# Performance work log

Measured on AMD Instinct MI355X. Metric: run time of the kernel, lower is better.

Reference implementation:

```python
import jax, jax.numpy as jnp
import numpy as np

D_MODEL = 1024
NHEAD = 16
DHEAD = D_MODEL // NHEAD
DFF = 4096
B, S = 2, 2048
R = 25                # local_attention_radius = 5*5
K = 5                 # rel_pos_max_distance
W = 2 * R + 1         # window width
EPS = 1e-5


def setup_inputs() -> dict:
    key = jax.random.key(0)
    ks = jax.random.split(key, 12)
    s = 0.02
    g = lambda k, shape: jax.random.normal(k, shape, jnp.float32) * s
    return {
        "src": jax.random.normal(ks[0], (B, S, D_MODEL), jnp.float32),
        # attention in/out projections (W stored [out,in], applied x @ W.T + b)
        "wq": g(ks[1], (D_MODEL, D_MODEL)), "bq": jnp.zeros((D_MODEL,), jnp.float32),
        "wk": g(ks[2], (D_MODEL, D_MODEL)), "bk": jnp.zeros((D_MODEL,), jnp.float32),
        "wv": g(ks[3], (D_MODEL, D_MODEL)), "bv": jnp.zeros((D_MODEL,), jnp.float32),
        "wo": g(ks[4], (D_MODEL, D_MODEL)), "bo": jnp.zeros((D_MODEL,), jnp.float32),
        # relative position embeddings, ids clipped to [-K, K] -> 2K+1 rows
        "rel_emb": g(ks[5], (2 * K + 1, DHEAD)),
        # FFN
        "w1": g(ks[6], (DFF, D_MODEL)), "b1": jnp.zeros((DFF,), jnp.float32),
        "w2": g(ks[7], (D_MODEL, DFF)), "b2": jnp.zeros((D_MODEL,), jnp.float32),
        # layernorms
        "g1": jnp.ones((D_MODEL,), jnp.float32), "beta1": jnp.zeros((D_MODEL,), jnp.float32),
        "g2": jnp.ones((D_MODEL,), jnp.float32), "beta2": jnp.zeros((D_MODEL,), jnp.float32),
    }


def _layernorm(x, g, b):
    m = x.mean(-1, keepdims=True)
    v = ((x - m) ** 2).mean(-1, keepdims=True)
    return (x - m) * jax.lax.rsqrt(v + EPS) * g + b


def _rel_window_attention(x, wq, bq, wk, bk, wv, bv, wo, bo, rel_emb):
    b, s, d = x.shape

    def proj(w, bias):
        return (x @ w.T + bias).reshape(b, s, NHEAD, DHEAD).transpose(0, 2, 1, 3)

    q = proj(wq, bq)  # [B,H,S,Dh]
    k = proj(wk, bk)
    v = proj(wv, bv)

    offsets = jnp.arange(-R, R + 1)                     # [W]
    j = jnp.arange(s)[:, None] + offsets[None, :]       # [S,W] absolute key index
    valid = (j >= 0) & (j < s)
    jc = jnp.clip(j, 0, s - 1)

    scale = 1.0 / np.sqrt(DHEAD).astype(np.float32)
    k_win = k[:, :, jc]                                 # [B,H,S,W,Dh] banded gather
    scores = jnp.einsum('bhsd,bhswd->bhsw', q, k_win) * scale
    rel_ids = jnp.clip(offsets, -K, K) + K              # [W]
    scores = scores + jnp.einsum('bhsd,wd->bhsw', q, rel_emb[rel_ids]) * scale
    scores = jnp.where(valid[None, None], scores, jnp.float32(-1e30))
    attn = jax.nn.softmax(scores, axis=-1)              # [B,H,S,W]

    v_win = v[:, :, jc]                                 # [B,H,S,W,Dh]
    out = jnp.einsum('bhsw,bhswd->bhsd', attn, v_win)
    out = out.transpose(0, 2, 1, 3).reshape(b, s, d)
    return out @ wo.T + bo


def reference(src, wq, bq, wk, bk, wv, bv, wo, bo, rel_emb,
              w1, b1, w2, b2, g1, beta1, g2, beta2):
    # post-norm (norm_first=False default) transformer block, dropout=0 (eval)
    z = _rel_window_attention(src, wq, bq, wk, bk, wv, bv, wo, bo, rel_emb)
    x = _layernorm(src + z, g1, beta1)
    ff = jax.nn.relu(x @ w1.T + b1) @ w2.T + b2
    return _layernorm(x + ff, g2, beta2)
```

## Files before the change

kernel.cpp:

```cpp
#include <hip/hip_runtime.h>


#define D_MODEL 1024
#define SEQ     2048
#define NROWS   4096
#define WIN     51
#define RAD     25

typedef __attribute__((ext_vector_type(8))) __bf16 bf16x8;
typedef __attribute__((ext_vector_type(4))) float  floatx4;

__device__ __forceinline__ unsigned short f2bf(float x) {
    unsigned u = __float_as_uint(x);
    unsigned r = u + 0x7fffu + ((u >> 16) & 1u);
    return (unsigned short)(r >> 16);
}
__device__ __forceinline__ float bf2f(unsigned short h) {
    return __uint_as_float(((unsigned)h) << 16);
}

__device__ __forceinline__ void gld16(const unsigned short* g, unsigned short* l) {
    __builtin_amdgcn_global_load_lds(
        (const __attribute__((address_space(1))) unsigned int*)g,
        (__attribute__((address_space(3))) unsigned int*)l,
        16, 0, 0);
}

__device__ __forceinline__ void cvtgrp(const float* __restrict__ in,
                                       unsigned short* __restrict__ out, int g) {
    float4 f = ((const float4*)in)[g];
    ushort4 u;
    u.x = f2bf(f.x); u.y = f2bf(f.y); u.z = f2bf(f.z); u.w = f2bf(f.w);
    ((ushort4*)out)[g] = u;
}

__global__ __launch_bounds__(256)
void cvt_all(const float* __restrict__ src,
             const float* __restrict__ wq, const float* __restrict__ wk,
             const float* __restrict__ wv, const float* __restrict__ wo,
             const float* __restrict__ w1, const float* __restrict__ w2,
             const float* __restrict__ bq, const float* __restrict__ bk,
             const float* __restrict__ bv,
             unsigned short* __restrict__ xb,
             unsigned short* __restrict__ wqkvb,
             unsigned short* __restrict__ wob,
             unsigned short* __restrict__ w1b,
             unsigned short* __restrict__ w2b,
             float* __restrict__ bqkv)
{
    int g = blockIdx.x * 256 + threadIdx.x;
    if (g >= 4194496) return;
    if (g < 1048576) { cvtgrp(src, xb, g); return; }
    g -= 1048576;
    if (g < 262144) { cvtgrp(wq, wqkvb, g); return; }
    g -= 262144;
    if (g < 262144) { cvtgrp(wk, wqkvb + 1048576, g); return; }
    g -= 262144;
    if (g < 262144) { cvtgrp(wv, wqkvb + 2097152, g); return; }
    g -= 262144;
    if (g < 262144) { cvtgrp(wo, wob, g); return; }
    g -= 262144;
    if (g < 1048576) { cvtgrp(w1, w1b, g); return; }
    g -= 1048576;
    if (g < 1048576) { cvtgrp(w2, w2b, g); return; }
    g -= 1048576;
    float4 f = (g < 64) ? ((const float4*)bq)[g]
             : (g < 128) ? ((const float4*)bk)[g - 64]
                         : ((const float4*)bv)[g - 128];
    ((float4*)bqkv)[g] = f;
}

#define ROT3(x) ((x) == 16384 ? 0 : (x) + 8192)

__global__ __launch_bounds__(512, 2)
void gemm256(const unsigned short* __restrict__ A,
             const unsigned short* __restrict__ Wt,
             const float* __restrict__ bias,
             unsigned short* __restrict__ Cb,
             int kstride, int kloop, int T, int tncnt,
             int ldc, int relu, size_t sstep1, size_t sstep2)
{
    __shared__ __attribute__((aligned(16))) unsigned short AS[3 * 8192];
    __shared__ __attribute__((aligned(16))) unsigned short BS[3 * 8192];

    const int id = blockIdx.x;
    const int s  = id / T;
    const int t0 = id - s * T;
    const int sid = (t0 & 7) * (T >> 3) + (t0 >> 3);
    const int bm = (sid / tncnt) * 256;
    const int bn = (sid % tncnt) * 256;

    const int tid  = threadIdx.x;
    const int lane = tid & 63;
    const int wave = tid >> 6;
    const int wr   = wave >> 2;
    const int wc   = wave & 3;
    const int fm   = lane & 15;
    const int fq   = lane >> 4;

    const int kofs = s * kloop;
    const int NT   = kloop >> 5;

    const int ks  = (tid >> 3) & 7;
    const int gi  = tid ^ ks;
    const int r0s = gi >> 2;
    const int c2s = gi & 3;
    const unsigned short* Agp = A  + (size_t)(bm + r0s) * kstride + kofs + c2s * 8;
    const unsigned short* Wgp = Wt + (size_t)(bn + r0s) * kstride + kofs + c2s * 8;
    const size_t istep = (size_t)128 * kstride;

    const int rA  = wr * 128 + fm;
    const int rB  = wc * 64  + fm;
    const int c0A = ((((rA << 2) | fq) ^ (fm >> 1)) << 3);
    const int c0B = ((((rB << 2) | fq) ^ (fm >> 1)) << 3);

    gld16(Agp,              AS + tid * 8);
    gld16(Agp + istep,      AS + tid * 8 + 4096);
    gld16(Wgp,              BS + tid * 8);
    gld16(Wgp + istep,      BS + tid * 8 + 4096);
    gld16(Agp + 32,         AS + 8192 + tid * 8);
    gld16(Agp + 32 + istep, AS + 8192 + tid * 8 + 4096);
    gld16(Wgp + 32,         BS + 8192 + tid * 8);
    gld16(Wgp + 32 + istep, BS + 8192 + tid * 8 + 4096);
    asm volatile("s_waitcnt vmcnt(4)" ::: "memory");
    __builtin_amdgcn_sched_barrier(0);
    __builtin_amdgcn_s_barrier();
    __builtin_amdgcn_sched_barrier(0);

    floatx4 acc[8][4] = {};
    const unsigned short* Aga = Agp + 64;
    const unsigned short* Wga = Wgp + 64;
    int cb = 0;
    int pb = 16384;

    for (int t = 0; t < NT; t++) {
        const bool pf = (t + 2 < NT);

        bf16x8 af0[4], bfr[4];
        #pragma unroll
        for (int mi = 0; mi < 4; mi++)
            af0[mi] = *(const bf16x8*)(AS + cb + c0A + mi * 512);
        #pragma unroll
        for (int ni = 0; ni < 4; ni++)
            bfr[ni] = *(const bf16x8*)(BS + cb + c0B + ni * 512);
        if (pf) {
            gld16(Aga,         AS + pb + tid * 8);
            gld16(Aga + istep, AS + pb + tid * 8 + 4096);
        }
        __builtin_amdgcn_sched_barrier(0);
        __builtin_amdgcn_s_barrier();
        __builtin_amdgcn_sched_barrier(0);
        __builtin_amdgcn_s_setprio(1);
        #pragma unroll
        for (int mi = 0; mi < 4; mi++)
            #pragma unroll
            for (int ni = 0; ni < 4; ni++)
                acc[mi][ni] = __builtin_amdgcn_mfma_f32_16x16x32_bf16(
                    af0[mi], bfr[ni], acc[mi][ni], 0, 0, 0);
        __builtin_amdgcn_s_setprio(0);
        __builtin_amdgcn_sched_barrier(0);
        __builtin_amdgcn_s_barrier();
        __builtin_amdgcn_sched_barrier(0);

        bf16x8 af1[4];
        #pragma unroll
        for (int mi = 0; mi < 4; mi++)
            af1[mi] = *(const bf16x8*)(AS + cb + c0A + (mi + 4) * 512);
        if (pf) {
            gld16(Wga,         BS + pb + tid * 8);
            gld16(Wga + istep, BS + pb + tid * 8 + 4096);
        }
        __builtin_amdgcn_sched_barrier(0);
        __builtin_amdgcn_s_barrier();
        __builtin_amdgcn_sched_barrier(0);
        __builtin_amdgcn_s_setprio(1);
        #pragma unroll
        for (int mi = 0; mi < 4; mi++)
            #pragma unroll
            for (int ni = 0; ni < 4; ni++)
                acc[mi + 4][ni] = __builtin_amdgcn_mfma_f32_16x16x32_bf16(
                    af1[mi], bfr[ni], acc[mi + 4][ni], 0, 0, 0);
        __builtin_amdgcn_s_setprio(0);

        if (t + 1 < NT) {
            if (pf) asm volatile("s_waitcnt vmcnt(4)" ::: "memory");
            else    asm volatile("s_waitcnt vmcnt(0)" ::: "memory");
            __builtin_amdgcn_sched_barrier(0);
            __builtin_amdgcn_s_barrier();
            __builtin_amdgcn_sched_barrier(0);
        }
        cb = ROT3(cb);
        pb = ROT3(pb);
        Aga += 32;
        Wga += 32;
    }

    unsigned short* Co = Cb + (size_t)(s & 1) * sstep1 + (size_t)(s >> 1) * sstep2;
    const int r0  = bm + wr * 128 + fq * 4;
    const int c0e = bn + wc * 64 + fm;
    #pragma unroll
    for (int mi = 0; mi < 8; mi++) {
        #pragma unroll
        for (int ni = 0; ni < 4; ni++) {
            const int col = c0e + ni * 16;
            const float bv = bias ? bias[col] : 0.0f;
            #pragma unroll
            for (int rr = 0; rr < 4; rr++) {
                const int row = r0 + mi * 16 + rr;
                float v = acc[mi][ni][rr] + bv;
                if (relu) v = fmaxf(v, 0.0f);
                Co[(size_t)row * ldc + col] = f2bf(v);
            }
        }
    }
}

__global__ __launch_bounds__(256, 2)
void attn_mfma(const unsigned short* __restrict__ qkv,
               const float* __restrict__ rel,
               unsigned short* __restrict__ attnb)
{
    __shared__ __attribute__((aligned(16))) unsigned short Qs[64 * 72];
    __shared__ __attribute__((aligned(16))) unsigned short Ks[128 * 72];
    __shared__ __attribute__((aligned(16))) unsigned short Vt[64 * 168];
    __shared__ __attribute__((aligned(16))) unsigned short Rs[16 * 72];
    __shared__ __attribute__((aligned(16))) unsigned short Pl[4 * 16 * 104];
    __shared__ float Qrl[4 * 16 * 12];

    const int t   = threadIdx.x;
    const int blk = blockIdx.x;
    const int st  = blk & 31;
    const int h   = (blk >> 5) & 15;
    const int b   = blk >> 9;
    const int s0  = st << 6;
    const int brow0 = b * SEQ;

    const int trow = t >> 3;
    const int tc   = (t & 7) * 8;
    const uint4 z4 = make_uint4(0, 0, 0, 0);

    #pragma unroll
    for (int p = 0; p < 2; p++) {
        int r = trow + p * 32;
        uint4 v = *(const uint4*)(qkv + (size_t)(brow0 + s0 + r) * 3072 + h * 64 + tc);
        *(uint4*)(Qs + r * 72 + tc) = v;
    }
    #pragma unroll
    for (int p = 0; p < 4; p++) {
        int kr = trow + p * 32;
        int ka = s0 - 25 + kr;
        bool in = (ka >= 0) & (ka < SEQ);
        uint4 kv = z4, vv = z4;
        if (in) {
            kv = *(const uint4*)(qkv + (size_t)(brow0 + ka) * 3072 + 1024 + h * 64 + tc);
            vv = *(const uint4*)(qkv + (size_t)(brow0 + ka) * 3072 + 2048 + h * 64 + tc);
        }
        *(uint4*)(Ks + kr * 72 + tc) = kv;
        const unsigned short* e = (const unsigned short*)&vv;
        #pragma unroll
        for (int j = 0; j < 8; j++)
            Vt[(tc + j) * 168 + kr] = e[j];
    }
    if (t < 176) {
        float4 f = ((const float4*)rel)[t];
        int fi = t * 4, rr = fi >> 6, cc = fi & 63;
        ushort4 u;
        u.x = f2bf(f.x); u.y = f2bf(f.y); u.z = f2bf(f.z); u.w = f2bf(f.w);
        *(ushort4*)(Rs + rr * 72 + cc) = u;
    } else {
        int fi = 704 + (t - 176) * 4, rr = fi >> 6, cc = fi & 63;
        *(ushort4*)(Rs + rr * 72 + cc) = make_ushort4(0, 0, 0, 0);
    }
    {
        int n = t * 4, w2 = n >> 8, rem = n & 255, rr = rem >> 4, cc = 80 + (rem & 15);
        *(ushort4*)(Pl + w2 * (16 * 104) + rr * 104 + cc) = make_ushort4(0, 0, 0, 0);
    }
    for (int idx = t; idx < 320; idx += 256) {
        int r = idx / 5, cchunk = idx % 5;
        *(uint4*)(Vt + r * 168 + 128 + cchunk * 8) = z4;
    }
    __syncthreads();

    const int wave = t >> 6;
    const int lane = t & 63;
    const int fm   = lane & 15;
    const int fk8  = (lane >> 4) * 8;
    const int S0w  = s0 + wave * 16;
    unsigned short* Plw = Pl + wave * (16 * 104);
    float* Ql = Qrl + wave * (16 * 12);

    bf16x8 qa0 = *(const bf16x8*)(Qs + (wave * 16 + fm) * 72 + fk8);
    bf16x8 qa1 = *(const bf16x8*)(Qs + (wave * 16 + fm) * 72 + fk8 + 32);

    floatx4 Sc[5];
    #pragma unroll
    for (int nt = 0; nt < 5; nt++) {
        bf16x8 kb0 = *(const bf16x8*)(Ks + (wave * 16 + nt * 16 + fm) * 72 + fk8);
        bf16x8 kb1 = *(const bf16x8*)(Ks + (wave * 16 + nt * 16 + fm) * 72 + fk8 + 32);
        floatx4 acc = {0.f, 0.f, 0.f, 0.f};
        acc = __builtin_amdgcn_mfma_f32_16x16x32_bf16(qa0, kb0, acc, 0, 0, 0);
        acc = __builtin_amdgcn_mfma_f32_16x16x32_bf16(qa1, kb1, acc, 0, 0, 0);
        Sc[nt] = acc;
    }
    {
        bf16x8 rb0 = *(const bf16x8*)(Rs + fm * 72 + fk8);
        bf16x8 rb1 = *(const bf16x8*)(Rs + fm * 72 + fk8 + 32);
        floatx4 qr = {0.f, 0.f, 0.f, 0.f};
        qr = __builtin_amdgcn_mfma_f32_16x16x32_bf16(qa0, rb0, qr, 0, 0, 0);
        qr = __builtin_amdgcn_mfma_f32_16x16x32_bf16(qa1, rb1, qr, 0, 0, 0);
        if (fm < 12) {
            #pragma unroll
            for (int reg = 0; reg < 4; reg++)
                Ql[((lane >> 4) * 4 + reg) * 12 + fm] = qr[reg];
        }
    }

    float inv[4];
    const int iq0 = (lane >> 4) * 4;
    #pragma unroll
    for (int reg = 0; reg < 4; reg++) {
        const int i = iq0 + reg;
        float sc[5];
        float mx = -1e30f;
        #pragma unroll
        for (int nt = 0; nt < 5; nt++) {
            int c   = nt * 16 + fm;
            int off = c - 25 - i;
            int ka  = S0w - 25 + c;
            bool valid = (off >= -RAD) & (off <= RAD) & (ka >= 0) & (ka < SEQ);
            int rid = min(max(off, -5), 5) + 5;
            float v = valid ? (Sc[nt][reg] + Ql[i * 12 + rid]) * 0.125f : -1e30f;
            sc[nt] = v;
            mx = fmaxf(mx, v);
        }
        #pragma unroll
        for (int o = 1; o < 16; o <<= 1) mx = fmaxf(mx, __shfl_xor(mx, o));
        float sum = 0.f;
        #pragma unroll
        for (int nt = 0; nt < 5; nt++) {
            float e = __expf(sc[nt] - mx);
            sum += e;
            Plw[i * 104 + nt * 16 + fm] = f2bf(e);
        }
        #pragma unroll
        for (int o = 1; o < 16; o <<= 1) sum += __shfl_xor(sum, o);
        inv[reg] = 1.0f / sum;
    }

    floatx4 O[4] = {};
    #pragma unroll
    for (int kc = 0; kc < 3; kc++) {
        bf16x8 pa = *(const bf16x8*)(Plw + fm * 104 + fk8 + kc * 32);
        #pragma unroll
        for (int nt = 0; nt < 4; nt++) {
            bf16x8 vb = *(const bf16x8*)(Vt + (nt * 16 + fm) * 168 + wave * 16 + fk8 + kc * 32);
            O[nt] = __builtin_amdgcn_mfma_f32_16x16x32_bf16(pa, vb, O[nt], 0, 0, 0);
        }
    }

    #pragma unroll
    for (int nt = 0; nt < 4; nt++) {
        const int d = nt * 16 + fm;
        #pragma unroll
        for (int reg = 0; reg < 4; reg++) {
            const int i = iq0 + reg;
            attnb[(size_t)(brow0 + S0w + i) * 1024 + h * 64 + d] = f2bf(O[nt][reg] * inv[reg]);
        }
    }
}

__global__ __launch_bounds__(256)
void ln_fuse(const float* __restrict__ resf,
             const unsigned short* __restrict__ resb,
             const unsigned short* __restrict__ p0,
             const unsigned short* __restrict__ p1,
             const unsigned short* __restrict__ p2,
             const unsigned short* __restrict__ p3,
             const float* __restrict__ cbias,
             const float* __restrict__ gamma,
             const float* __restrict__ beta,
             float* __restrict__ outf,
             unsigned short* __restrict__ outb)
{
    const int wave = threadIdx.x >> 6;
    const int lane = threadIdx.x & 63;
    const int row = blockIdx.x * 4 + wave;
    const size_t base = (size_t)row * D_MODEL;

    float x[16];
    float sum = 0.0f, sq = 0.0f;
    #pragma unroll
    for (int i = 0; i < 4; i++) {
        const int c4 = lane + i * 64;
        ushort4 u0 = ((const ushort4*)(p0 + base))[c4];
        ushort4 u1 = ((const ushort4*)(p1 + base))[c4];
        float4 cb = ((const float4*)cbias)[c4];
        float4 va;
        if (resf) {
            va = ((const float4*)(resf + base))[c4];
        } else {
            ushort4 ua = ((const ushort4*)(resb + base))[c4];
            va.x = bf2f(ua.x); va.y = bf2f(ua.y); va.z = bf2f(ua.z); va.w = bf2f(ua.w);
        }
        float e0 = va.x + bf2f(u0.x) + bf2f(u1.x) + cb.x;
        float e1 = va.y + bf2f(u0.y) + bf2f(u1.y) + cb.y;
        float e2 = va.z + bf2f(u0.z) + bf2f(u1.z) + cb.z;
        float e3 = va.w + bf2f(u0.w) + bf2f(u1.w) + cb.w;
        if (p2) {
            ushort4 u2 = ((const ushort4*)(p2 + base))[c4];
            ushort4 u3 = ((const ushort4*)(p3 + base))[c4];
            e0 += bf2f(u2.x) + bf2f(u3.x);
            e1 += bf2f(u2.y) + bf2f(u3.y);
            e2 += bf2f(u2.z) + bf2f(u3.z);
            e3 += bf2f(u2.w) + bf2f(u3.w);
        }
        x[i*4+0] = e0; x[i*4+1] = e1; x[i*4+2] = e2; x[i*4+3] = e3;
        sum += e0 + e1 + e2 + e3;
        sq  += e0*e0 + e1*e1 + e2*e2 + e3*e3;
    }
    #pragma unroll
    for (int off = 32; off > 0; off >>= 1) {
        sum += __shfl_xor(sum, off);
        sq  += __shfl_xor(sq,  off);
    }
    const float mean = sum * (1.0f / 1024.0f);
    const float var  = sq  * (1.0f / 1024.0f) - mean * mean;
    const float rs   = rsqrtf(var + 1e-5f);

    #pragma unroll
    for (int i = 0; i < 4; i++) {
        const int c4 = lane + i * 64;
        float4 g4 = ((const float4*)gamma)[c4];
        float4 b4 = ((const float4*)beta)[c4];
        float4 o;
        o.x = (x[i*4+0] - mean) * rs * g4.x + b4.x;
        o.y = (x[i*4+1] - mean) * rs * g4.y + b4.y;
        o.z = (x[i*4+2] - mean) * rs * g4.z + b4.z;
        o.w = (x[i*4+3] - mean) * rs * g4.w + b4.w;
        if (outf) ((float4*)(outf + base))[c4] = o;
        if (outb) {
            ushort4 u;
            u.x = f2bf(o.x); u.y = f2bf(o.y); u.z = f2bf(o.z); u.w = f2bf(o.w);
            ((ushort4*)(outb + base))[c4] = u;
        }
    }
}

extern "C" void kernel_launch(void* const* d_in, const int* in_sizes, int n_in,
                              void* d_out, int out_size, void* d_ws, size_t ws_size,
                              hipStream_t stream)
{
    const float* src = (const float*)d_in[0];
    const float* wq  = (const float*)d_in[1];
    const float* bq  = (const float*)d_in[2];
    const float* wk  = (const float*)d_in[3];
    const float* bk  = (const float*)d_in[4];
    const float* wv  = (const float*)d_in[5];
    const float* bv  = (const float*)d_in[6];
    const float* wo  = (const float*)d_in[7];
    const float* bo  = (const float*)d_in[8];
    const float* rel = (const float*)d_in[9];
    const float* w1  = (const float*)d_in[10];
    const float* b1  = (const float*)d_in[11];
    const float* w2  = (const float*)d_in[12];
    const float* b2  = (const float*)d_in[13];
    const float* g1  = (const float*)d_in[14];
    const float* be1 = (const float*)d_in[15];
    const float* g2  = (const float*)d_in[16];
    const float* be2 = (const float*)d_in[17];
    float* out = (float*)d_out;

    char* ws = (char*)d_ws;
    const size_t MB = 1048576;
    unsigned short* wqkvb = (unsigned short*)(ws + 0);
    unsigned short* wob   = (unsigned short*)(ws + 6  * MB);
    unsigned short* w1b   = (unsigned short*)(ws + 8  * MB);
    unsigned short* w2b   = (unsigned short*)(ws + 16 * MB);
    float*          bqkv  = (float*)         (ws + 24 * MB);
    unsigned short* xb    = (unsigned short*)(ws + 25 * MB);
    unsigned short* attnb = xb;
    unsigned short* qkvb  = (unsigned short*)(ws + 33 * MB);
    unsigned short* z01   = (unsigned short*)(ws + 33 * MB);
    unsigned short* x1b   = (unsigned short*)(ws + 49 * MB);
    unsigned short* ff1b  = (unsigned short*)(ws + 57 * MB);
    unsigned short* f01   = (unsigned short*)(ws + 0);
    const size_t SL    = (size_t)NROWS * 1024;
    const size_t SOFF2 = (size_t)12 * MB;

    const dim3 blk(256);
    const dim3 blk5(512);
    cvt_all<<<16385, blk, 0, stream>>>(src, wq, wk, wv, wo, w1, w2, bq, bk, bv,
                                       xb, wqkvb, wob, w1b, w2b, bqkv);
    gemm256<<<192, blk5, 0, stream>>>(xb, wqkvb, bqkv, qkvb, 1024, 1024, 192, 12,
                                      3072, 0, 0, 0);
    attn_mfma<<<1024, blk, 0, stream>>>(qkvb, rel, attnb);
    gemm256<<<256, blk5, 0, stream>>>(attnb, wob, nullptr, z01, 1024, 256, 64, 4,
                                      1024, 0, SL, SOFF2);
    ln_fuse<<<NROWS / 4, blk, 0, stream>>>(src, nullptr, z01, z01 + SL,
                                           z01 + SOFF2, z01 + SOFF2 + SL,
                                           bo, g1, be1, nullptr, x1b);
    gemm256<<<256, blk5, 0, stream>>>(x1b, w1b, b1, ff1b, 1024, 1024, 256, 16,
                                      4096, 1, 0, 0);
    gemm256<<<256, blk5, 0, stream>>>(ff1b, w2b, nullptr, f01, 4096, 1024, 64, 4,
                                      1024, 0, SL, SOFF2);
    ln_fuse<<<NROWS / 4, blk, 0, stream>>>(nullptr, x1b, f01, f01 + SL,
                                           f01 + SOFF2, f01 + SOFF2 + SL,
                                           b2, g2, be2, out, nullptr);
}
```

Before: 312.2 us.

## Switch GEMMs to 256x128 tiles with 4-wave blocks and fewer barriers

Replaces the 512-thread 256x256-tile GEMM with a 256-thread kernel computing 256x128 tiles. Each wave now owns a 128x64 sub-tile and loads all eight A fragments at once. The two half-step barrier phases per k-iteration are merged into a single one, and grids double to give more blocks per GEMM. The goal is less intra-block synchronisation and better CU fill, at the cost of lower arithmetic intensity per tile and more register pressure from holding eight A fragments.

After: 307.5 us. No clear change (-1.5%).

```diff
diff --git a/kernel.cpp b/kernel.cpp
--- a/kernel.cpp
+++ b/kernel.cpp
@@ -70,10 +70,8 @@
     ((float4*)bqkv)[g] = f;
 }
 
-#define ROT3(x) ((x) == 16384 ? 0 : (x) + 8192)
-
-__global__ __launch_bounds__(512, 2)
-void gemm256(const unsigned short* __restrict__ A,
+__global__ __launch_bounds__(256, 2)
+void gemm_dp(const unsigned short* __restrict__ A,
              const unsigned short* __restrict__ Wt,
              const float* __restrict__ bias,
              unsigned short* __restrict__ Cb,
@@ -81,20 +79,20 @@
              int ldc, int relu, size_t sstep1, size_t sstep2)
 {
     __shared__ __attribute__((aligned(16))) unsigned short AS[3 * 8192];
-    __shared__ __attribute__((aligned(16))) unsigned short BS[3 * 8192];
+    __shared__ __attribute__((aligned(16))) unsigned short BS[3 * 4096];
 
     const int id = blockIdx.x;
     const int s  = id / T;
     const int t0 = id - s * T;
     const int sid = (t0 & 7) * (T >> 3) + (t0 >> 3);
     const int bm = (sid / tncnt) * 256;
-    const int bn = (sid % tncnt) * 256;
+    const int bn = (sid % tncnt) * 128;
 
     const int tid  = threadIdx.x;
     const int lane = tid & 63;
     const int wave = tid >> 6;
-    const int wr   = wave >> 2;
-    const int wc   = wave & 3;
+    const int wr   = wave >> 1;
+    const int wc   = wave & 1;
     const int fm   = lane & 15;
     const int fq   = lane >> 4;
 
@@ -107,22 +105,31 @@
     const int c2s = gi & 3;
     const unsigned short* Agp = A  + (size_t)(bm + r0s) * kstride + kofs + c2s * 8;
     const unsigned short* Wgp = Wt + (size_t)(bn + r0s) * kstride + kofs + c2s * 8;
-    const size_t istep = (size_t)128 * kstride;
+    const size_t istep = (size_t)64 * kstride;
 
     const int rA  = wr * 128 + fm;
     const int rB  = wc * 64  + fm;
     const int c0A = ((((rA << 2) | fq) ^ (fm >> 1)) << 3);
     const int c0B = ((((rB << 2) | fq) ^ (fm >> 1)) << 3);
 
-    gld16(Agp,              AS + tid * 8);
-    gld16(Agp + istep,      AS + tid * 8 + 4096);
-    gld16(Wgp,              BS + tid * 8);
-    gld16(Wgp + istep,      BS + tid * 8 + 4096);
-    gld16(Agp + 32,         AS + 8192 + tid * 8);
-    gld16(Agp + 32 + istep, AS + 8192 + tid * 8 + 4096);
-    gld16(Wgp + 32,         BS + 8192 + tid * 8);
-    gld16(Wgp + 32 + istep, BS + 8192 + tid * 8 + 4096);
-    asm volatile("s_waitcnt vmcnt(4)" ::: "memory");
+    {
+        const unsigned short* Ap = Agp;
+        const unsigned short* Wp = Wgp;
+        gld16(Ap,             AS + tid * 8);
+        gld16(Ap + istep,     AS + tid * 8 + 2048);
+        gld16(Ap + 2 * istep, AS + tid * 8 + 4096);
+        gld16(Ap + 3 * istep, AS + tid * 8 + 6144);
+        gld16(Wp,             BS + tid * 8);
+        gld16(Wp + istep,     BS + tid * 8 + 2048);
+        Ap += 32; Wp += 32;
+        gld16(Ap,             AS + 8192 + tid * 8);
+        gld16(Ap + istep,     AS + 8192 + tid * 8 + 2048);
+        gld16(Ap + 2 * istep, AS + 8192 + tid * 8 + 4096);
+        gld16(Ap + 3 * istep, AS + 8192 + tid * 8 + 6144);
+        gld16(Wp,             BS + 4096 + tid * 8);
+        gld16(Wp + istep,     BS + 4096 + tid * 8 + 2048);
+    }
+    asm volatile("s_waitcnt vmcnt(6)" ::: "memory");
     __builtin_amdgcn_sched_barrier(0);
     __builtin_amdgcn_s_barrier();
     __builtin_amdgcn_sched_barrier(0);
@@ -130,67 +137,49 @@
     floatx4 acc[8][4] = {};
     const unsigned short* Aga = Agp + 64;
     const unsigned short* Wga = Wgp + 64;
-    int cb = 0;
-    int pb = 16384;
+    int cbA = 0, cbB = 0;
+    int pbA = 16384, pbB = 8192;
 
     for (int t = 0; t < NT; t++) {
         const bool pf = (t + 2 < NT);
 
-        bf16x8 af0[4], bfr[4];
-        #pragma unroll
-        for (int mi = 0; mi < 4; mi++)
-            af0[mi] = *(const bf16x8*)(AS + cb + c0A + mi * 512);
+        bf16x8 af[8], bf[4];
+        #pragma unroll
+        for (int mi = 0; mi < 8; mi++)
+            af[mi] = *(const bf16x8*)(AS + cbA + c0A + mi * 512);
         #pragma unroll
         for (int ni = 0; ni < 4; ni++)
-            bfr[ni] = *(const bf16x8*)(BS + cb + c0B + ni * 512);
+            bf[ni] = *(const bf16x8*)(BS + cbB + c0B + ni * 512);
+
         if (pf) {
-            gld16(Aga,         AS + pb + tid * 8);
-            gld16(Aga + istep, AS + pb + tid * 8 + 4096);
-        }
-        __builtin_amdgcn_sched_barrier(0);
-        __builtin_amdgcn_s_barrier();
-        __builtin_amdgcn_sched_barrier(0);
+            gld16(Aga,             AS + pbA + tid * 8);
+            gld16(Aga + istep,     AS + pbA + tid * 8 + 2048);
+            gld16(Aga + 2 * istep, AS + pbA + tid * 8 + 4096);
+            gld16(Aga + 3 * istep, AS + pbA + tid * 8 + 6144);
+            gld16(Wga,             BS + pbB + tid * 8);
+            gld16(Wga + istep,     BS + pbB + tid * 8 + 2048);
+        }
+
         __builtin_amdgcn_s_setprio(1);
         #pragma unroll
-        for (int mi = 0; mi < 4; mi++)
+        for (int mi = 0; mi < 8; mi++)
             #pragma unroll
             for (int ni = 0; ni < 4; ni++)
                 acc[mi][ni] = __builtin_amdgcn_mfma_f32_16x16x32_bf16(
-                    af0[mi], bfr[ni], acc[mi][ni], 0, 0, 0);
+                    af[mi], bf[ni], acc[mi][ni], 0, 0, 0);
         __builtin_amdgcn_s_setprio(0);
-        __builtin_amdgcn_sched_barrier(0);
-        __builtin_amdgcn_s_barrier();
-        __builtin_amdgcn_sched_barrier(0);
-
-        bf16x8 af1[4];
-        #pragma unroll
-        for (int mi = 0; mi < 4; mi++)
-            af1[mi] = *(const bf16x8*)(AS + cb + c0A + (mi + 4) * 512);
-        if (pf) {
-            gld16(Wga,         BS + pb + tid * 8);
-            gld16(Wga + istep, BS + pb + tid * 8 + 4096);
-        }
-        __builtin_amdgcn_sched_barrier(0);
-        __builtin_amdgcn_s_barrier();
-        __builtin_amdgcn_sched_barrier(0);
-        __builtin_amdgcn_s_setprio(1);
-        #pragma unroll
-        for (int mi = 0; mi < 4; mi++)
-            #pragma unroll
-            for (int ni = 0; ni < 4; ni++)
-                acc[mi + 4][ni] = __builtin_amdgcn_mfma_f32_16x16x32_bf16(
-                    af1[mi], bfr[ni], acc[mi + 4][ni], 0, 0, 0);
-        __builtin_amdgcn_s_setprio(0);
 
         if (t + 1 < NT) {
-            if (pf) asm volatile("s_waitcnt vmcnt(4)" ::: "memory");
+            if (pf) asm volatile("s_waitcnt vmcnt(6)" ::: "memory");
             else    asm volatile("s_waitcnt vmcnt(0)" ::: "memory");
             __builtin_amdgcn_sched_barrier(0);
             __builtin_amdgcn_s_barrier();
             __builtin_amdgcn_sched_barrier(0);
         }
-        cb = ROT3(cb);
-        pb = ROT3(pb);
+        cbA = (cbA == 16384) ? 0 : cbA + 8192;
+        cbB = (cbB == 8192)  ? 0 : cbB + 4096;
+        pbA = (pbA == 16384) ? 0 : pbA + 8192;
+        pbB = (pbB == 8192)  ? 0 : pbB + 4096;
         Aga += 32;
         Wga += 32;
     }
@@ -488,21 +477,20 @@
     const size_t SOFF2 = (size_t)12 * MB;
 
     const dim3 blk(256);
-    const dim3 blk5(512);
     cvt_all<<<16385, blk, 0, stream>>>(src, wq, wk, wv, wo, w1, w2, bq, bk, bv,
                                        xb, wqkvb, wob, w1b, w2b, bqkv);
-    gemm256<<<192, blk5, 0, stream>>>(xb, wqkvb, bqkv, qkvb, 1024, 1024, 192, 12,
-                                      3072, 0, 0, 0);
+    gemm_dp<<<384, blk, 0, stream>>>(xb, wqkvb, bqkv, qkvb, 1024, 1024, 384, 24,
+                                     3072, 0, 0, 0);
     attn_mfma<<<1024, blk, 0, stream>>>(qkvb, rel, attnb);
-    gemm256<<<256, blk5, 0, stream>>>(attnb, wob, nullptr, z01, 1024, 256, 64, 4,
-                                      1024, 0, SL, SOFF2);
+    gemm_dp<<<512, blk, 0, stream>>>(attnb, wob, nullptr, z01, 1024, 256, 128, 8,
+                                     1024, 0, SL, SOFF2);
     ln_fuse<<<NROWS / 4, blk, 0, stream>>>(src, nullptr, z01, z01 + SL,
                                            z01 + SOFF2, z01 + SOFF2 + SL,
                                            bo, g1, be1, nullptr, x1b);
-    gemm256<<<256, blk5, 0, stream>>>(x1b, w1b, b1, ff1b, 1024, 1024, 256, 16,
-                                      4096, 1, 0, 0);
-    gemm256<<<256, blk5, 0, stream>>>(ff1b, w2b, nullptr, f01, 4096, 1024, 64, 4,
-                                      1024, 0, SL, SOFF2);
+    gemm_dp<<<512, blk, 0, stream>>>(x1b, w1b, b1, ff1b, 1024, 1024, 512, 32,
+                                     4096, 1, 0, 0);
+    gemm_dp<<<512, blk, 0, stream>>>(ff1b, w2b, nullptr, f01, 4096, 1024, 128, 8,
+                                     1024, 0, SL, SOFF2);
     ln_fuse<<<NROWS / 4, blk, 0, stream>>>(nullptr, x1b, f01, f01 + SL,
                                            f01 + SOFF2, f01 + SOFF2 + SL,
                                            b2, g2, be2, out, nullptr);
```

## Restructure GEMM into double-buffered K=64 eight-phase ping-pong pipeline

Applied to the files above, without the earlier changes.

Replaces the triple-buffered K=32 GEMM main loop with a double-buffered K=64 stage, splitting each stage into four MFMA quadrant phases that interleave LDS reads, async global->LDS prefetches and barriers. Each iteration processes two K=64 stages (128 of K). The aim is to amortize barrier and load-issue overhead over more MFMA work and to hide global latency better. It raises LDS use per block to 128 KB, which may limit occupancy, and relies on careful vmcnt accounting.

New measurement: 307.4 us. About the same (-1.6%).

```diff
diff --git a/kernel.cpp b/kernel.cpp
--- a/kernel.cpp
+++ b/kernel.cpp
@@ -70,22 +70,20 @@
     ((float4*)bqkv)[g] = f;
 }
 
-#define ROT3(x) ((x) == 16384 ? 0 : (x) + 8192)
-
 __global__ __launch_bounds__(512, 2)
-void gemm256(const unsigned short* __restrict__ A,
-             const unsigned short* __restrict__ Wt,
-             const float* __restrict__ bias,
-             unsigned short* __restrict__ Cb,
-             int kstride, int kloop, int T, int tncnt,
-             int ldc, int relu, size_t sstep1, size_t sstep2)
+void gemm8p(const unsigned short* __restrict__ A,
+            const unsigned short* __restrict__ Wt,
+            const float* __restrict__ bias,
+            unsigned short* __restrict__ Cb,
+            int kstride, int kloop, int T, int tncnt,
+            int ldc, int relu, size_t sstep1, size_t sstep2)
 {
-    __shared__ __attribute__((aligned(16))) unsigned short AS[3 * 8192];
-    __shared__ __attribute__((aligned(16))) unsigned short BS[3 * 8192];
+    __shared__ __attribute__((aligned(16))) unsigned short AS[2 * 16384];
+    __shared__ __attribute__((aligned(16))) unsigned short BS[2 * 16384];
 
     const int id = blockIdx.x;
-    const int s  = id / T;
-    const int t0 = id - s * T;
+    const int sl = id / T;
+    const int t0 = id - sl * T;
     const int sid = (t0 & 7) * (T >> 3) + (t0 >> 3);
     const int bm = (sid / tncnt) * 256;
     const int bn = (sid % tncnt) * 256;
@@ -98,104 +96,120 @@
     const int fm   = lane & 15;
     const int fq   = lane >> 4;
 
-    const int kofs = s * kloop;
-    const int NT   = kloop >> 5;
-
-    const int ks  = (tid >> 3) & 7;
-    const int gi  = tid ^ ks;
-    const int r0s = gi >> 2;
-    const int c2s = gi & 3;
-    const unsigned short* Agp = A  + (size_t)(bm + r0s) * kstride + kofs + c2s * 8;
-    const unsigned short* Wgp = Wt + (size_t)(bn + r0s) * kstride + kofs + c2s * 8;
-    const size_t istep = (size_t)128 * kstride;
-
-    const int rA  = wr * 128 + fm;
-    const int rB  = wc * 64  + fm;
-    const int c0A = ((((rA << 2) | fq) ^ (fm >> 1)) << 3);
-    const int c0B = ((((rB << 2) | fq) ^ (fm >> 1)) << 3);
-
-    gld16(Agp,              AS + tid * 8);
-    gld16(Agp + istep,      AS + tid * 8 + 4096);
-    gld16(Wgp,              BS + tid * 8);
-    gld16(Wgp + istep,      BS + tid * 8 + 4096);
-    gld16(Agp + 32,         AS + 8192 + tid * 8);
-    gld16(Agp + 32 + istep, AS + 8192 + tid * 8 + 4096);
-    gld16(Wgp + 32,         BS + 8192 + tid * 8);
-    gld16(Wgp + 32 + istep, BS + 8192 + tid * 8 + 4096);
+    const int kofs  = sl * kloop;
+    const int NITER = kloop >> 7;
+
+    const int srow = tid >> 3;
+    const int scol = ((tid & 7) ^ ((tid >> 3) & 7)) * 8;
+    const unsigned short* PA = A  + (size_t)(bm + srow) * kstride + kofs + scol;
+    const unsigned short* PW = Wt + (size_t)(bn + srow) * kstride + kofs + scol;
+    const size_t rs64 = (size_t)64 * kstride;
+
+    const int aoff = (wr * 128 + fm) * 64;
+    const int boff = (wc * 64  + fm) * 64;
+    const int ck0  = (fq ^ (fm & 7)) * 8;
+    const int ck1  = ck0 ^ 32;
+
+    floatx4 acc[8][4] = {};
+
+    auto STG = [&](const unsigned short* g, int h, unsigned short* l) {
+        gld16(g + (size_t)(2 * h)     * rs64, l + h * 8192 + tid * 8);
+        gld16(g + (size_t)(2 * h + 1) * rs64, l + h * 8192 + 4096 + tid * 8);
+    };
+    auto rdA = [&](bf16x8 (&d)[4][2], int bufb, int mb) {
+        #pragma unroll
+        for (int mi = 0; mi < 4; mi++) {
+            d[mi][0] = *(const bf16x8*)(AS + bufb + aoff + (mb + mi) * 1024 + ck0);
+            d[mi][1] = *(const bf16x8*)(AS + bufb + aoff + (mb + mi) * 1024 + ck1);
+        }
+    };
+    auto rdB = [&](bf16x8 (&d)[2][2], int bufb, int nb) {
+        #pragma unroll
+        for (int ni = 0; ni < 2; ni++) {
+            d[ni][0] = *(const bf16x8*)(BS + bufb + boff + (nb + ni) * 1024 + ck0);
+            d[ni][1] = *(const bf16x8*)(BS + bufb + boff + (nb + ni) * 1024 + ck1);
+        }
+    };
+    auto mmq = [&](bf16x8 (&a)[4][2], bf16x8 (&b)[2][2], int mb, int nb) {
+        __builtin_amdgcn_s_setprio(1);
+        #pragma unroll
+        for (int ks = 0; ks < 2; ks++)
+            #pragma unroll
+            for (int mi = 0; mi < 4; mi++)
+                #pragma unroll
+                for (int ni = 0; ni < 2; ni++)
+                    acc[mb + mi][nb + ni] = __builtin_amdgcn_mfma_f32_16x16x32_bf16(
+                        a[mi][ks], b[ni][ks], acc[mb + mi][nb + ni], 0, 0, 0);
+        __builtin_amdgcn_s_setprio(0);
+    };
+    auto barpre = [&]() {
+        __builtin_amdgcn_sched_barrier(0);
+        __builtin_amdgcn_s_barrier();
+        asm volatile("s_waitcnt lgkmcnt(0)" ::: "memory");
+        __builtin_amdgcn_sched_barrier(0);
+    };
+    auto barpost = [&]() {
+        __builtin_amdgcn_sched_barrier(0);
+        __builtin_amdgcn_s_barrier();
+        __builtin_amdgcn_sched_barrier(0);
+    };
+
+    unsigned short* AS0 = AS;            unsigned short* AS1 = AS + 16384;
+    unsigned short* BS0 = BS;            unsigned short* BS1 = BS + 16384;
+
+    STG(PA, 0, AS0); STG(PA, 1, AS0);
+    STG(PW, 0, BS0); STG(PW, 1, BS0);
+    STG(PW + 64, 0, BS1); STG(PW + 64, 1, BS1);
+    __builtin_amdgcn_sched_barrier(0);
     asm volatile("s_waitcnt vmcnt(4)" ::: "memory");
     __builtin_amdgcn_sched_barrier(0);
     __builtin_amdgcn_s_barrier();
     __builtin_amdgcn_sched_barrier(0);
 
-    floatx4 acc[8][4] = {};
-    const unsigned short* Aga = Agp + 64;
-    const unsigned short* Wga = Wgp + 64;
-    int cb = 0;
-    int pb = 16384;
-
-    for (int t = 0; t < NT; t++) {
-        const bool pf = (t + 2 < NT);
-
-        bf16x8 af0[4], bfr[4];
-        #pragma unroll
-        for (int mi = 0; mi < 4; mi++)
-            af0[mi] = *(const bf16x8*)(AS + cb + c0A + mi * 512);
-        #pragma unroll
-        for (int ni = 0; ni < 4; ni++)
-            bfr[ni] = *(const bf16x8*)(BS + cb + c0B + ni * 512);
-        if (pf) {
-            gld16(Aga,         AS + pb + tid * 8);
-            gld16(Aga + istep, AS + pb + tid * 8 + 4096);
-        }
+    for (int it = 0; it < NITER; it++) {
+        const bool more = (it + 1 < NITER);
+        bf16x8 a03[4][2], a47[4][2], b01[2][2], b23[2][2];
+
+        rdA(a03, 0, 0); rdB(b01, 0, 0);
+        STG(PA + 64, 0, AS1);
+        barpre(); mmq(a03, b01, 0, 0); barpost();
+        rdB(b23, 0, 2);
+        STG(PA + 64, 1, AS1);
+        barpre(); mmq(a03, b23, 0, 2); barpost();
+        rdA(a47, 0, 4);
+        if (more) STG(PW + 128, 0, BS0);
+        barpre(); mmq(a47, b01, 4, 0); barpost();
+        if (more) STG(PW + 128, 1, BS0);
+        __builtin_amdgcn_sched_barrier(0);
+        if (more) asm volatile("s_waitcnt vmcnt(4)" ::: "memory");
+        else      asm volatile("s_waitcnt vmcnt(0)" ::: "memory");
         __builtin_amdgcn_sched_barrier(0);
         __builtin_amdgcn_s_barrier();
         __builtin_amdgcn_sched_barrier(0);
-        __builtin_amdgcn_s_setprio(1);
-        #pragma unroll
-        for (int mi = 0; mi < 4; mi++)
-            #pragma unroll
-            for (int ni = 0; ni < 4; ni++)
-                acc[mi][ni] = __builtin_amdgcn_mfma_f32_16x16x32_bf16(
-                    af0[mi], bfr[ni], acc[mi][ni], 0, 0, 0);
-        __builtin_amdgcn_s_setprio(0);
+        mmq(a47, b23, 4, 2); barpost();
+        rdA(a03, 16384, 0); rdB(b01, 16384, 0);
+        if (more) STG(PA + 128, 0, AS0);
+        barpre(); mmq(a03, b01, 0, 0); barpost();
+        rdB(b23, 16384, 2);
+        if (more) STG(PA + 128, 1, AS0);
+        barpre(); mmq(a03, b23, 0, 2); barpost();
+        rdA(a47, 16384, 4);
+        if (more) STG(PW + 192, 0, BS1);
+        barpre(); mmq(a47, b01, 4, 0); barpost();
+        if (more) {
+            STG(PW + 192, 1, BS1);
+            __builtin_amdgcn_sched_barrier(0);
+            asm volatile("s_waitcnt vmcnt(4)" ::: "memory");
+        }
         __builtin_amdgcn_sched_barrier(0);
         __builtin_amdgcn_s_barrier();
         __builtin_amdgcn_sched_barrier(0);
-
-        bf16x8 af1[4];
-        #pragma unroll
-        for (int mi = 0; mi < 4; mi++)
-            af1[mi] = *(const bf16x8*)(AS + cb + c0A + (mi + 4) * 512);
-        if (pf) {
-            gld16(Wga,         BS + pb + tid * 8);
-            gld16(Wga + istep, BS + pb + tid * 8 + 4096);
-        }
-        __builtin_amdgcn_sched_barrier(0);
-        __builtin_amdgcn_s_barrier();
-        __builtin_amdgcn_sched_barrier(0);
-        __builtin_amdgcn_s_setprio(1);
-        #pragma unroll
-        for (int mi = 0; mi < 4; mi++)
-            #pragma unroll
-            for (int ni = 0; ni < 4; ni++)
-                acc[mi + 4][ni] = __builtin_amdgcn_mfma_f32_16x16x32_bf16(
-                    af1[mi], bfr[ni], acc[mi + 4][ni], 0, 0, 0);
-        __builtin_amdgcn_s_setprio(0);
-
-        if (t + 1 < NT) {
-            if (pf) asm volatile("s_waitcnt vmcnt(4)" ::: "memory");
-            else    asm volatile("s_waitcnt vmcnt(0)" ::: "memory");
-            __builtin_amdgcn_sched_barrier(0);
-            __builtin_amdgcn_s_barrier();
-            __builtin_amdgcn_sched_barrier(0);
-        }
-        cb = ROT3(cb);
-        pb = ROT3(pb);
-        Aga += 32;
-        Wga += 32;
-    }
-
-    unsigned short* Co = Cb + (size_t)(s & 1) * sstep1 + (size_t)(s >> 1) * sstep2;
+        mmq(a47, b23, 4, 2); barpost();
+
+        PA += 128; PW += 128;
+    }
+
+    unsigned short* Co = Cb + (size_t)(sl & 1) * sstep1 + (size_t)(sl >> 1) * sstep2;
     const int r0  = bm + wr * 128 + fq * 4;
     const int c0e = bn + wc * 64 + fm;
     #pragma unroll
@@ -491,18 +505,18 @@
     const dim3 blk5(512);
     cvt_all<<<16385, blk, 0, stream>>>(src, wq, wk, wv, wo, w1, w2, bq, bk, bv,
                                        xb, wqkvb, wob, w1b, w2b, bqkv);
-    gemm256<<<192, blk5, 0, stream>>>(xb, wqkvb, bqkv, qkvb, 1024, 1024, 192, 12,
-                                      3072, 0, 0, 0);
+    gemm8p<<<192, blk5, 0, stream>>>(xb, wqkvb, bqkv, qkvb, 1024, 1024, 192, 12,
+                                     3072, 0, 0, 0);
     attn_mfma<<<1024, blk, 0, stream>>>(qkvb, rel, attnb);
-    gemm256<<<256, blk5, 0, stream>>>(attnb, wob, nullptr, z01, 1024, 256, 64, 4,
-                                      1024, 0, SL, SOFF2);
+    gemm8p<<<256, blk5, 0, stream>>>(attnb, wob, nullptr, z01, 1024, 256, 64, 4,
+                                     1024, 0, SL, SOFF2);
     ln_fuse<<<NROWS / 4, blk, 0, stream>>>(src, nullptr, z01, z01 + SL,
                                            z01 + SOFF2, z01 + SOFF2 + SL,
                                            bo, g1, be1, nullptr, x1b);
-    gemm256<<<256, blk5, 0, stream>>>(x1b, w1b, b1, ff1b, 1024, 1024, 256, 16,
-                                      4096, 1, 0, 0);
-    gemm256<<<256, blk5, 0, stream>>>(ff1b, w2b, nullptr, f01, 4096, 1024, 64, 4,
-                                      1024, 0, SL, SOFF2);
+    gemm8p<<<256, blk5, 0, stream>>>(x1b, w1b, b1, ff1b, 1024, 1024, 256, 16,
+                                     4096, 1, 0, 0);
+    gemm8p<<<256, blk5, 0, stream>>>(ff1b, w2b, nullptr, f01, 4096, 1024, 64, 4,
+                                     1024, 0, SL, SOFF2);
     ln_fuse<<<NROWS / 4, blk, 0, stream>>>(nullptr, x1b, f01, f01 + SL,
                                            f01 + SOFF2, f01 + SOFF2 + SL,
                                            b2, g2, be2, out, nullptr);
```
